# Performance work log

Hardware: AMD Instinct MI355X
Metric: run time of the kernel (lower is better)

Reference implementation:

```python
import jax, jax.numpy as jnp
import numpy as np


def setup_inputs() -> dict:
    key = jax.random.key(0)
    k1, k2, k3, k4 = jax.random.split(key, 4)
    B, T, C, H = 16, 2048, 1024, 128
    x = jax.random.normal(k1, (B, T, C), dtype=jnp.float32)
    # bias-free Dense kernels (stored as [in, out] like keras)
    s = 1.0 / np.sqrt(C)
    Wk = jax.random.normal(k2, (C, H), dtype=jnp.float32) * s
    Wq = jax.random.normal(k3, (C, H), dtype=jnp.float32) * s
    Wv = jax.random.normal(k4, (C, H), dtype=jnp.float32) * s
    return {"x": x, "Wk": Wk, "Wq": Wq, "Wv": Wv}


def reference(x, Wk, Wq, Wv):
    # single-head causal self-attention (dropout inactive at inference)
    B, T, C = x.shape
    H = Wk.shape[-1]
    k = jnp.einsum('btc,ch->bth', x, Wk)   # [B,T,H]
    q = jnp.einsum('btc,ch->bth', x, Wq)
    v = jnp.einsum('btc,ch->bth', x, Wv)
    scale = 1.0 / jnp.sqrt(jnp.float32(H))
    wei = jnp.einsum('bqh,bkh->bqk', q, k) * scale          # [B,T,T]
    causal = jnp.tril(jnp.ones((T, T), dtype=bool))
    wei = jnp.where(causal, wei, -jnp.inf)
    wei = jax.nn.softmax(wei, axis=-1)
    out = jnp.einsum('bqk,bkh->bqh', wei, v)                # [B,T,H]
    return out
```

## Files before the change

### kernel.cpp

```cpp
#include <hip/hip_runtime.h>
#include <hip/hip_bf16.h>

typedef __bf16 bf16x8_t __attribute__((ext_vector_type(8)));
typedef __bf16 bf16x4_t __attribute__((ext_vector_type(4)));
typedef float  f32x4_t  __attribute__((ext_vector_type(4)));

#define MFMA_16x16x32_BF16(A, B, C) __builtin_amdgcn_mfma_f32_16x16x32_bf16((A), (B), (C), 0, 0, 0)

static constexpr int B_ = 16;
static constexpr int T_ = 2048;
static constexpr int C_ = 1024;
static constexpr int H_ = 128;
static constexpr long M_ = (long)B_ * T_;

__global__ __launch_bounds__(128) void wt_kernel(
    const float* __restrict__ Wq, const float* __restrict__ Wk,
    const float* __restrict__ Wv, __bf16* __restrict__ WT)
{
    const int z = blockIdx.y;
    const float* __restrict__ W = (z == 0) ? Wq : (z == 1) ? Wk : Wv;
    const int h  = threadIdx.x;
    const int c0 = blockIdx.x * 8;
    bf16x8_t v;
    #pragma unroll
    for (int j = 0; j < 8; ++j)
        v[j] = (__bf16)W[(c0 + j) * H_ + h];
    *(bf16x8_t*)&WT[((long)z * H_ + h) * C_ + c0] = v;
}

__global__ __launch_bounds__(256) void proj_kernel(
    const float*  __restrict__ x,
    const __bf16* __restrict__ WT,
    __bf16* __restrict__ qo,
    __bf16* __restrict__ ko,
    __bf16* __restrict__ vo)
{
    __shared__ __bf16 XS[64 * 40];
    __shared__ __bf16 WS[384 * 40];

    const int tid  = threadIdx.x;
    const int lane = tid & 63;
    const int w    = tid >> 6;
    const int m16  = lane & 15;
    const int quad = lane >> 4;
    const int koff = quad * 8;

    const long r0 = (long)blockIdx.x * 64;

    f32x4_t acc[24];
    #pragma unroll
    for (int nt = 0; nt < 24; ++nt) acc[nt] = f32x4_t{0, 0, 0, 0};

    for (int k0 = 0; k0 < C_; k0 += 32) {
        #pragma unroll
        for (int ch = 0; ch < 2; ++ch) {
            int s   = tid + 256 * ch;
            int row = s >> 3, c = s & 7;
            f32x4_t xv = *(const f32x4_t*)&x[(r0 + row) * C_ + k0 + c * 4];
            bf16x4_t xb;
            #pragma unroll
            for (int j = 0; j < 4; ++j) xb[j] = (__bf16)xv[j];
            *(bf16x4_t*)&XS[row * 40 + c * 4] = xb;
        }
        #pragma unroll
        for (int ch = 0; ch < 6; ++ch) {
            int g = tid + 256 * ch;
            int n = g >> 2, kc = g & 3;
            *(bf16x8_t*)&WS[n * 40 + kc * 8] =
                *(const bf16x8_t*)&WT[(long)n * C_ + k0 + kc * 8];
        }
        __syncthreads();

        bf16x8_t a = *(const bf16x8_t*)&XS[(w * 16 + m16) * 40 + koff];
        #pragma unroll
        for (int nt = 0; nt < 24; ++nt) {
            bf16x8_t bfr = *(const bf16x8_t*)&WS[(nt * 16 + m16) * 40 + koff];
            acc[nt] = MFMA_16x16x32_BF16(a, bfr, acc[nt]);
        }
        __syncthreads();
    }

    const long rbase = r0 + w * 16 + quad * 4;
    #pragma unroll
    for (int nt = 0; nt < 24; ++nt) {
        int z = nt >> 3;
        int h = (nt & 7) * 16 + m16;
        if (z < 2) {
            __bf16* __restrict__ o = z ? ko : qo;
            #pragma unroll
            for (int r = 0; r < 4; ++r)
                o[(rbase + r) * H_ + h] = (__bf16)acc[nt][r];
        } else {
            long bb = rbase >> 11, tt = rbase & 2047;
            bf16x4_t pk;
            #pragma unroll
            for (int r = 0; r < 4; ++r) pk[r] = (__bf16)acc[nt][r];
            *(bf16x4_t*)&vo[bb * (H_ * (long)T_) + h * (long)T_ + tt] = pk;
        }
    }
}

__global__ __launch_bounds__(256) void attn_kernel(
    const __bf16* __restrict__ q,
    const __bf16* __restrict__ k,
    const __bf16* __restrict__ vT,
    float* __restrict__ out)
{
    __shared__ __bf16 KS[64 * 136];
    __shared__ __bf16 VS[128 * 72];
    __shared__ __bf16 PS[4][16 * 72];

    const int L   = blockIdx.x;
    const int b   = L & 15;
    const int Lh  = L >> 4;
    const int qb  = (Lh < 16) ? (31 - Lh) : (Lh - 16);

    const int tid  = threadIdx.x;
    const int w    = tid >> 6;
    const int lane = tid & 63;
    const int m16  = lane & 15;
    const int quad = lane >> 4;
    const int koff = quad * 8;

    const __bf16* __restrict__ qp = q  + (long)b * T_ * H_;
    const __bf16* __restrict__ kp = k  + (long)b * T_ * H_;
    const __bf16* __restrict__ vp = vT + (long)b * H_ * T_;

    const int q0w = qb * 64 + w * 16;
    const int qg  = q0w + m16;

    bf16x8_t qfr[4];
    #pragma unroll
    for (int s = 0; s < 4; ++s)
        qfr[s] = *(const bf16x8_t*)&qp[(q0w + m16) * H_ + s * 32 + koff];

    f32x4_t acc[8];
    #pragma unroll
    for (int i = 0; i < 8; ++i) acc[i] = f32x4_t{0, 0, 0, 0};
    float mrun = -1e30f, lrun = 0.f;

    __bf16* Pb = &PS[w][0];
    const float SC = 0.08838834764831845f;
    const int kend = qb * 64 + 64;

    const int krow = tid >> 4, kc16 = tid & 15;
    const int vrow = tid >> 3, vc8  = tid & 7;

    for (int tk0 = 0; tk0 < kend; tk0 += 64) {
        __syncthreads();
        #pragma unroll
        for (int ch = 0; ch < 4; ++ch) {
            int r = krow + ch * 16;
            *(bf16x8_t*)&KS[r * 136 + kc16 * 8] =
                *(const bf16x8_t*)&kp[(tk0 + r) * H_ + kc16 * 8];
        }
        #pragma unroll
        for (int ch = 0; ch < 4; ++ch) {
            int hh = vrow + ch * 32;
            *(bf16x8_t*)&VS[hh * 72 + vc8 * 8] =
                *(const bf16x8_t*)&vp[hh * (long)T_ + tk0 + vc8 * 8];
        }
        __syncthreads();

        f32x4_t st[4];
        #pragma unroll
        for (int kt = 0; kt < 4; ++kt) {
            f32x4_t s = f32x4_t{0, 0, 0, 0};
            #pragma unroll
            for (int sI = 0; sI < 4; ++sI) {
                bf16x8_t kf = *(const bf16x8_t*)&KS[(kt * 16 + m16) * 136 + sI * 32 + koff];
                s = MFMA_16x16x32_BF16(kf, qfr[sI], s);
            }
            st[kt] = s;
        }

        float vv[4][4];
        if (tk0 + 63 <= q0w) {
            #pragma unroll
            for (int kt = 0; kt < 4; ++kt)
                #pragma unroll
                for (int r = 0; r < 4; ++r)
                    vv[kt][r] = st[kt][r] * SC;
        } else {
            #pragma unroll
            for (int kt = 0; kt < 4; ++kt)
                #pragma unroll
                for (int r = 0; r < 4; ++r) {
                    int kg = tk0 + kt * 16 + quad * 4 + r;
                    vv[kt][r] = (kg <= qg) ? st[kt][r] * SC : -1e30f;
                }
        }

        float mloc = -1e30f;
        #pragma unroll
        for (int kt = 0; kt < 4; ++kt)
            #pragma unroll
            for (int r = 0; r < 4; ++r)
                mloc = fmaxf(mloc, vv[kt][r]);
        mloc = fmaxf(mloc, __shfl_xor(mloc, 16, 64));
        mloc = fmaxf(mloc, __shfl_xor(mloc, 32, 64));

        float mnew = fmaxf(mrun, mloc);
        float al   = __expf(mrun - mnew);
        float psum = 0.f;
        #pragma unroll
        for (int kt = 0; kt < 4; ++kt) {
            bf16x4_t pk;
            #pragma unroll
            for (int r = 0; r < 4; ++r) {
                float p = __expf(vv[kt][r] - mnew);
                psum += p;
                pk[r] = (__bf16)p;
            }
            *(bf16x4_t*)&Pb[m16 * 72 + kt * 16 + quad * 4] = pk;
        }
        psum += __shfl_xor(psum, 16, 64);
        psum += __shfl_xor(psum, 32, 64);
        mrun = mnew;
        lrun = lrun * al + psum;

        #pragma unroll
        for (int i = 0; i < 8; ++i)
            #pragma unroll
            for (int r = 0; r < 4; ++r)
                acc[i][r] *= al;

        #pragma unroll
        for (int half = 0; half < 2; ++half) {
            bf16x8_t pa = *(const bf16x8_t*)&Pb[m16 * 72 + half * 32 + koff];
            #pragma unroll
            for (int i = 0; i < 8; ++i) {
                bf16x8_t vf = *(const bf16x8_t*)&VS[(i * 16 + m16) * 72 + half * 32 + koff];
                acc[i] = MFMA_16x16x32_BF16(vf, pa, acc[i]);
            }
        }
    }

    float* __restrict__ ob = out + (long)b * T_ * H_;
    const float inv = 1.f / lrun;
    #pragma unroll
    for (int i = 0; i < 8; ++i) {
        f32x4_t o;
        #pragma unroll
        for (int r = 0; r < 4; ++r) o[r] = acc[i][r] * inv;
        *(f32x4_t*)&ob[(q0w + m16) * H_ + i * 16 + quad * 4] = o;
    }
}

extern "C" void kernel_launch(void* const* d_in, const int* in_sizes, int n_in,
                              void* d_out, int out_size, void* d_ws, size_t ws_size,
                              hipStream_t stream)
{
    const float* x  = (const float*)d_in[0];
    const float* Wk = (const float*)d_in[1];
    const float* Wq = (const float*)d_in[2];
    const float* Wv = (const float*)d_in[3];

    __bf16* qws = (__bf16*)d_ws;
    __bf16* kws = qws + M_ * H_;
    __bf16* vws = kws + M_ * H_;
    __bf16* WT  = vws + (long)B_ * H_ * T_;
    float*  out = (float*)d_out;

    wt_kernel  <<<dim3(C_ / 8, 3), 128, 0, stream>>>(Wq, Wk, Wv, WT);
    proj_kernel<<<dim3((int)(M_ / 64)), 256, 0, stream>>>(x, WT, qws, kws, vws);
    attn_kernel<<<dim3(512), 256, 0, stream>>>(qws, kws, vws, out);
}
```

Before: 274.4 us.

## Double-buffer projection GEMM with direct global-to-LDS weight loads and 512 threads

The projection kernel now double-buffers the X and W tiles in shared memory. The next k-slice's loads are issued before the current MFMAs, so only one barrier per iteration is needed. Weight tiles go straight into LDS through global_load_lds, skipping registers. The block grows to 8 waves, each handling 16 rows by 12 N-tiles instead of 24, which cuts accumulator registers. In exchange, the LDS rows lose their padding, so bank conflicts may increase, and LDS use doubles.

```diff
diff --git a/kernel.cpp b/kernel.cpp
--- a/kernel.cpp
+++ b/kernel.cpp
@@ -13,6 +13,13 @@
 static constexpr int H_ = 128;
 static constexpr long M_ = (long)B_ * T_;
 
+__device__ __forceinline__ void gload_lds16(const void* g, void* l)
+{
+    __builtin_amdgcn_global_load_lds(
+        (const __attribute__((address_space(1))) void*)g,
+        (__attribute__((address_space(3))) void*)l, 16, 0, 0);
+}
+
 __global__ __launch_bounds__(128) void wt_kernel(
     const float* __restrict__ Wq, const float* __restrict__ Wk,
     const float* __restrict__ Wv, __bf16* __restrict__ WT)
@@ -28,92 +35,15 @@
     *(bf16x8_t*)&WT[((long)z * H_ + h) * C_ + c0] = v;
 }
 
-__global__ __launch_bounds__(256) void proj_kernel(
+__global__ __launch_bounds__(512, 4) void proj_kernel(
     const float*  __restrict__ x,
     const __bf16* __restrict__ WT,
     __bf16* __restrict__ qo,
     __bf16* __restrict__ ko,
     __bf16* __restrict__ vo)
 {
-    __shared__ __bf16 XS[64 * 40];
-    __shared__ __bf16 WS[384 * 40];
-
-    const int tid  = threadIdx.x;
-    const int lane = tid & 63;
-    const int w    = tid >> 6;
-    const int m16  = lane & 15;
-    const int quad = lane >> 4;
-    const int koff = quad * 8;
-
-    const long r0 = (long)blockIdx.x * 64;
-
-    f32x4_t acc[24];
-    #pragma unroll
-    for (int nt = 0; nt < 24; ++nt) acc[nt] = f32x4_t{0, 0, 0, 0};
-
-    for (int k0 = 0; k0 < C_; k0 += 32) {
-        #pragma unroll
-        for (int ch = 0; ch < 2; ++ch) {
-            int s   = tid + 256 * ch;
-            int row = s >> 3, c = s & 7;
-            f32x4_t xv = *(const f32x4_t*)&x[(r0 + row) * C_ + k0 + c * 4];
-            bf16x4_t xb;
-            #pragma unroll
-            for (int j = 0; j < 4; ++j) xb[j] = (__bf16)xv[j];
-            *(bf16x4_t*)&XS[row * 40 + c * 4] = xb;
-        }
-        #pragma unroll
-        for (int ch = 0; ch < 6; ++ch) {
-            int g = tid + 256 * ch;
-            int n = g >> 2, kc = g & 3;
-            *(bf16x8_t*)&WS[n * 40 + kc * 8] =
-                *(const bf16x8_t*)&WT[(long)n * C_ + k0 + kc * 8];
-        }
-        __syncthreads();
-
-        bf16x8_t a = *(const bf16x8_t*)&XS[(w * 16 + m16) * 40 + koff];
-        #pragma unroll
-        for (int nt = 0; nt < 24; ++nt) {
-            bf16x8_t bfr = *(const bf16x8_t*)&WS[(nt * 16 + m16) * 40 + koff];
-            acc[nt] = MFMA_16x16x32_BF16(a, bfr, acc[nt]);
-        }
-        __syncthreads();
-    }
-
-    const long rbase = r0 + w * 16 + quad * 4;
-    #pragma unroll
-    for (int nt = 0; nt < 24; ++nt) {
-        int z = nt >> 3;
-        int h = (nt & 7) * 16 + m16;
-        if (z < 2) {
-            __bf16* __restrict__ o = z ? ko : qo;
-            #pragma unroll
-            for (int r = 0; r < 4; ++r)
-                o[(rbase + r) * H_ + h] = (__bf16)acc[nt][r];
-        } else {
-            long bb = rbase >> 11, tt = rbase & 2047;
-            bf16x4_t pk;
-            #pragma unroll
-            for (int r = 0; r < 4; ++r) pk[r] = (__bf16)acc[nt][r];
-            *(bf16x4_t*)&vo[bb * (H_ * (long)T_) + h * (long)T_ + tt] = pk;
-        }
-    }
-}
-
-__global__ __launch_bounds__(256) void attn_kernel(
-    const __bf16* __restrict__ q,
-    const __bf16* __restrict__ k,
-    const __bf16* __restrict__ vT,
-    float* __restrict__ out)
-{
-    __shared__ __bf16 KS[64 * 136];
-    __shared__ __bf16 VS[128 * 72];
-    __shared__ __bf16 PS[4][16 * 72];
-
-    const int L   = blockIdx.x;
-    const int b   = L & 15;
-    const int Lh  = L >> 4;
-    const int qb  = (Lh < 16) ? (31 - Lh) : (Lh - 16);
+    __shared__ __bf16 XS[2][64 * 32];
+    __shared__ __bf16 WS[2][384 * 32];
 
     const int tid  = threadIdx.x;
     const int w    = tid >> 6;
@@ -121,6 +51,107 @@
     const int m16  = lane & 15;
     const int quad = lane >> 4;
     const int koff = quad * 8;
+    const int mt   = w >> 1;
+    const int nh   = w & 1;
+
+    const long r0 = (long)blockIdx.x * 64;
+
+    const int xrow = tid >> 3, xc = tid & 7;
+    const int wrow = lane >> 2, wcol = lane & 3;
+
+    f32x4_t acc[12];
+    #pragma unroll
+    for (int j = 0; j < 12; ++j) acc[j] = f32x4_t{0, 0, 0, 0};
+
+    {
+        f32x4_t xv = *(const f32x4_t*)&x[(r0 + xrow) * C_ + xc * 4];
+        #pragma unroll
+        for (int ch = 0; ch < 3; ++ch) {
+            const int rowb = w * 48 + ch * 16;
+            gload_lds16(&WT[(long)(rowb + wrow) * C_ + wcol * 8],
+                        &WS[0][rowb * 32]);
+        }
+        bf16x4_t xb;
+        #pragma unroll
+        for (int j = 0; j < 4; ++j) xb[j] = (__bf16)xv[j];
+        *(bf16x4_t*)&XS[0][xrow * 32 + xc * 4] = xb;
+    }
+    __syncthreads();
+
+    for (int t = 0; t < 32; ++t) {
+        const int cur = t & 1, nxt = cur ^ 1;
+        const int k0n = (t + 1) * 32;
+
+        f32x4_t xv;
+        if (t < 31) {
+            xv = *(const f32x4_t*)&x[(r0 + xrow) * C_ + k0n + xc * 4];
+            #pragma unroll
+            for (int ch = 0; ch < 3; ++ch) {
+                const int rowb = w * 48 + ch * 16;
+                gload_lds16(&WT[(long)(rowb + wrow) * C_ + k0n + wcol * 8],
+                            &WS[nxt][rowb * 32]);
+            }
+        }
+
+        bf16x8_t a = *(const bf16x8_t*)&XS[cur][(mt * 16 + m16) * 32 + koff];
+        #pragma unroll
+        for (int j = 0; j < 12; ++j) {
+            bf16x8_t bfr =
+                *(const bf16x8_t*)&WS[cur][((nh * 12 + j) * 16 + m16) * 32 + koff];
+            acc[j] = MFMA_16x16x32_BF16(a, bfr, acc[j]);
+        }
+
+        if (t < 31) {
+            bf16x4_t xb;
+            #pragma unroll
+            for (int j = 0; j < 4; ++j) xb[j] = (__bf16)xv[j];
+            *(bf16x4_t*)&XS[nxt][xrow * 32 + xc * 4] = xb;
+        }
+        __syncthreads();
+    }
+
+    const long rbase = r0 + mt * 16 + quad * 4;
+    #pragma unroll
+    for (int j = 0; j < 12; ++j) {
+        const int ntg = nh * 12 + j;
+        const int z = ntg >> 3;
+        const int h = (ntg & 7) * 16 + m16;
+        if (z < 2) {
+            __bf16* __restrict__ o = z ? ko : qo;
+            #pragma unroll
+            for (int r = 0; r < 4; ++r)
+                o[(rbase + r) * H_ + h] = (__bf16)acc[j][r];
+        } else {
+            long bb = rbase >> 11, tt = rbase & 2047;
+            bf16x4_t pk;
+            #pragma unroll
+            for (int r = 0; r < 4; ++r) pk[r] = (__bf16)acc[j][r];
+            *(bf16x4_t*)&vo[bb * (H_ * (long)T_) + h * (long)T_ + tt] = pk;
+        }
+    }
+}
+
+__global__ __launch_bounds__(256) void attn_kernel(
+    const __bf16* __restrict__ q,
+    const __bf16* __restrict__ k,
+    const __bf16* __restrict__ vT,
+    float* __restrict__ out)
+{
+    __shared__ __bf16 KS[64 * 136];
+    __shared__ __bf16 VS[128 * 72];
+    __shared__ __bf16 PS[4][16 * 72];
+
+    const int L   = blockIdx.x;
+    const int b   = L & 15;
+    const int Lh  = L >> 4;
+    const int qb  = (Lh < 16) ? (31 - Lh) : (Lh - 16);
+
+    const int tid  = threadIdx.x;
+    const int w    = tid >> 6;
+    const int lane = tid & 63;
+    const int m16  = lane & 15;
+    const int quad = lane >> 4;
+    const int koff = quad * 8;
 
     const __bf16* __restrict__ qp = q  + (long)b * T_ * H_;
     const __bf16* __restrict__ kp = k  + (long)b * T_ * H_;
@@ -263,6 +294,6 @@
     float*  out = (float*)d_out;
 
     wt_kernel  <<<dim3(C_ / 8, 3), 128, 0, stream>>>(Wq, Wk, Wv, WT);
-    proj_kernel<<<dim3((int)(M_ / 64)), 256, 0, stream>>>(x, WT, qws, kws, vws);
+    proj_kernel<<<dim3((int)(M_ / 64)), 512, 0, stream>>>(x, WT, qws, kws, vws);
     attn_kernel<<<dim3(512), 256, 0, stream>>>(qws, kws, vws, out);
 }
```

After: 291.9 us. 6.4% more time.

## Load projection operands directly into registers and drop LDS staging

Applied to the files above, without the earlier changes.

The projection kernel no longer stages x and W tiles in shared memory. Each wave now reads its A fragments straight from global memory (fp32 x converted to bf16 in registers) and its B fragments from WT, with x double-buffered in registers to overlap loads with MFMAs. Work is split so each wave owns 96 output columns across all 64 rows rather than 16 rows across all 384 columns. This removes the __syncthreads barriers and LDS traffic, but every wave now re-reads x from global/L2 (4x redundancy within a block) and raises register pressure, which the occupancy hint of 2 blocks per CU tries to bound.

```diff
diff --git a/kernel.cpp b/kernel.cpp
--- a/kernel.cpp
+++ b/kernel.cpp
@@ -28,74 +28,94 @@
     *(bf16x8_t*)&WT[((long)z * H_ + h) * C_ + c0] = v;
 }
 
-__global__ __launch_bounds__(256) void proj_kernel(
+__global__ __launch_bounds__(256, 2) void proj_kernel(
     const float*  __restrict__ x,
     const __bf16* __restrict__ WT,
     __bf16* __restrict__ qo,
     __bf16* __restrict__ ko,
     __bf16* __restrict__ vo)
 {
-    __shared__ __bf16 XS[64 * 40];
-    __shared__ __bf16 WS[384 * 40];
-
     const int tid  = threadIdx.x;
+    const int w    = tid >> 6;
     const int lane = tid & 63;
-    const int w    = tid >> 6;
     const int m16  = lane & 15;
     const int quad = lane >> 4;
-    const int koff = quad * 8;
 
     const long r0 = (long)blockIdx.x * 64;
 
-    f32x4_t acc[24];
-    #pragma unroll
-    for (int nt = 0; nt < 24; ++nt) acc[nt] = f32x4_t{0, 0, 0, 0};
-
-    for (int k0 = 0; k0 < C_; k0 += 32) {
-        #pragma unroll
-        for (int ch = 0; ch < 2; ++ch) {
-            int s   = tid + 256 * ch;
-            int row = s >> 3, c = s & 7;
-            f32x4_t xv = *(const f32x4_t*)&x[(r0 + row) * C_ + k0 + c * 4];
-            bf16x4_t xb;
-            #pragma unroll
-            for (int j = 0; j < 4; ++j) xb[j] = (__bf16)xv[j];
-            *(bf16x4_t*)&XS[row * 40 + c * 4] = xb;
-        }
-        #pragma unroll
-        for (int ch = 0; ch < 6; ++ch) {
-            int g = tid + 256 * ch;
-            int n = g >> 2, kc = g & 3;
-            *(bf16x8_t*)&WS[n * 40 + kc * 8] =
-                *(const bf16x8_t*)&WT[(long)n * C_ + k0 + kc * 8];
-        }
-        __syncthreads();
-
-        bf16x8_t a = *(const bf16x8_t*)&XS[(w * 16 + m16) * 40 + koff];
-        #pragma unroll
-        for (int nt = 0; nt < 24; ++nt) {
-            bf16x8_t bfr = *(const bf16x8_t*)&WS[(nt * 16 + m16) * 40 + koff];
-            acc[nt] = MFMA_16x16x32_BF16(a, bfr, acc[nt]);
-        }
-        __syncthreads();
-    }
-
-    const long rbase = r0 + w * 16 + quad * 4;
-    #pragma unroll
-    for (int nt = 0; nt < 24; ++nt) {
-        int z = nt >> 3;
-        int h = (nt & 7) * 16 + m16;
-        if (z < 2) {
-            __bf16* __restrict__ o = z ? ko : qo;
-            #pragma unroll
-            for (int r = 0; r < 4; ++r)
-                o[(rbase + r) * H_ + h] = (__bf16)acc[nt][r];
-        } else {
-            long bb = rbase >> 11, tt = rbase & 2047;
-            bf16x4_t pk;
-            #pragma unroll
-            for (int r = 0; r < 4; ++r) pk[r] = (__bf16)acc[nt][r];
-            *(bf16x4_t*)&vo[bb * (H_ * (long)T_) + h * (long)T_ + tt] = pk;
+    const float*  __restrict__ xb = x  + (r0 + m16) * C_ + quad * 8;
+    const __bf16* __restrict__ wb = WT + (long)(w * 96 + m16) * C_ + quad * 8;
+
+    f32x4_t acc[4][6];
+    #pragma unroll
+    for (int hh = 0; hh < 4; ++hh)
+        #pragma unroll
+        for (int j = 0; j < 6; ++j) acc[hh][j] = f32x4_t{0, 0, 0, 0};
+
+    f32x4_t xA[4][2], xB[4][2];
+
+    #pragma unroll
+    for (int hh = 0; hh < 4; ++hh) {
+        xA[hh][0] = *(const f32x4_t*)(xb + (long)hh * 16 * C_);
+        xA[hh][1] = *(const f32x4_t*)(xb + (long)hh * 16 * C_ + 4);
+    }
+
+#define PSTEP(T, XC, XN)                                                     \
+    {                                                                        \
+        const int t_  = (T);                                                 \
+        const int k0_ = t_ * 32;                                             \
+        bf16x8_t b_[6];                                                      \
+        _Pragma("unroll")                                                    \
+        for (int j = 0; j < 6; ++j)                                          \
+            b_[j] = *(const bf16x8_t*)(wb + (long)j * 16 * C_ + k0_);        \
+        if (t_ < 31) {                                                       \
+            _Pragma("unroll")                                                \
+            for (int hh = 0; hh < 4; ++hh) {                                 \
+                XN[hh][0] = *(const f32x4_t*)(xb + (long)hh * 16 * C_ + k0_ + 32); \
+                XN[hh][1] = *(const f32x4_t*)(xb + (long)hh * 16 * C_ + k0_ + 36); \
+            }                                                                \
+        }                                                                    \
+        bf16x8_t a_[4];                                                      \
+        _Pragma("unroll")                                                    \
+        for (int hh = 0; hh < 4; ++hh)                                       \
+            _Pragma("unroll")                                                \
+            for (int jj = 0; jj < 4; ++jj) {                                 \
+                a_[hh][jj]     = (__bf16)XC[hh][0][jj];                      \
+                a_[hh][4 + jj] = (__bf16)XC[hh][1][jj];                      \
+            }                                                                \
+        _Pragma("unroll")                                                    \
+        for (int j = 0; j < 6; ++j)                                          \
+            _Pragma("unroll")                                                \
+            for (int hh = 0; hh < 4; ++hh)                                   \
+                acc[hh][j] = MFMA_16x16x32_BF16(a_[hh], b_[j], acc[hh][j]);  \
+    }
+
+    for (int tp = 0; tp < 16; ++tp) {
+        PSTEP(2 * tp,     xA, xB);
+        PSTEP(2 * tp + 1, xB, xA);
+    }
+#undef PSTEP
+
+    #pragma unroll
+    for (int hh = 0; hh < 4; ++hh) {
+        const long rbase = r0 + hh * 16 + quad * 4;
+        #pragma unroll
+        for (int j = 0; j < 6; ++j) {
+            const int nt = w * 6 + j;
+            const int z  = nt >> 3;
+            const int h  = (nt & 7) * 16 + m16;
+            if (z < 2) {
+                __bf16* __restrict__ o = z ? ko : qo;
+                #pragma unroll
+                for (int r = 0; r < 4; ++r)
+                    o[(rbase + r) * H_ + h] = (__bf16)acc[hh][j][r];
+            } else {
+                long bb = rbase >> 11, tt = rbase & 2047;
+                bf16x4_t pk;
+                #pragma unroll
+                for (int r = 0; r < 4; ++r) pk[r] = (__bf16)acc[hh][j][r];
+                *(bf16x4_t*)&vo[bb * (H_ * (long)T_) + h * (long)T_ + tt] = pk;
+            }
         }
     }
 }
```

Result: slower. 330.1 us (+20.3%).
